# Kernel tuning notes

Hardware: AMD Instinct MI355X
Metric: run time of the kernel (lower is better)

## Reference

```python
import jax, jax.numpy as jnp
import numpy as np

EPS = 1e-5
H = 12  # num_heads

def ste_sign(x):
    # forward: sign(x) in {-1,+1}; backward: grad passes where |x|<1 (clip STE)
    c = jnp.clip(x, -1.0, 1.0)
    s = jnp.where(x >= 0, 1.0, -1.0).astype(x.dtype)
    return c + jax.lax.stop_gradient(s - c)

def bin_w(w):
    # adaptive per-output-channel scaling: alpha = mean|w| (detached), weight = alpha*sign(w)
    alpha = jax.lax.stop_gradient(jnp.mean(jnp.abs(w), axis=1, keepdims=True))
    return alpha * ste_sign(w)

def layernorm(x, g, b):
    mu = jnp.mean(x, axis=-1, keepdims=True)
    var = jnp.var(x, axis=-1, keepdims=True)
    return (x - mu) * jax.lax.rsqrt(var + EPS) * g + b

def setup_inputs():
    key = jax.random.key(0)
    ks = jax.random.split(key, 6)
    B, N, C, hid = 8, 1024, 768, 3072
    s = 0.02
    return {
        "x": jax.random.normal(ks[0], (B, N, C), jnp.float32),
        "ln1_g": jnp.ones((C,), jnp.float32),
        "ln1_b": jnp.zeros((C,), jnp.float32),
        "w_qkv": jax.random.normal(ks[1], (3 * C, C), jnp.float32) * s,
        "w_proj": jax.random.normal(ks[2], (C, C), jnp.float32) * s,
        "b_proj": jnp.zeros((C,), jnp.float32),
        "ls1_g": 1e-5 * jnp.ones((C,), jnp.float32),
        "ln2_g": jnp.ones((C,), jnp.float32),
        "ln2_b": jnp.zeros((C,), jnp.float32),
        "w_fc1": jax.random.normal(ks[3], (hid, C), jnp.float32) * s,
        "b_fc1": jnp.zeros((hid,), jnp.float32),
        "w_fc2": jax.random.normal(ks[4], (C, hid), jnp.float32) * s,
        "b_fc2": jnp.zeros((C,), jnp.float32),
        "ls2_g": 1e-5 * jnp.ones((C,), jnp.float32),
    }

def reference(x, ln1_g, ln1_b, w_qkv, w_proj, b_proj, ls1_g, ln2_g, ln2_b, w_fc1, b_fc1, w_fc2, b_fc2, ls2_g):
    B, N, C = x.shape
    hd = C // H
    scale = hd ** -0.5
    # --- binarized attention ---
    h = layernorm(x, ln1_g, ln1_b)
    qkv = jnp.einsum('bnc,oc->bno', ste_sign(h), bin_w(w_qkv))        # 1w1a qkv proj
    qkv = qkv.reshape(B, N, 3, H, hd).transpose(2, 0, 3, 1, 4)        # [3,B,H,N,hd]
    bqkv = ste_sign(qkv)                                              # BinaryQuantizer
    q, k, v = bqkv[0], bqkv[1], bqkv[2]
    attn = jnp.einsum('bhnd,bhmd->bhnm', q, k) * scale                # [B,H,N,N]
    sm = jax.nn.softmax(attn, axis=-1)
    abin = (attn > 0).astype(x.dtype)                                 # SoftmaxBinaryQuantizer fwd value
    attn_eff = sm + jax.lax.stop_gradient(abin - sm)                  # STE: fwd=binary, bwd=softmax
    o = jnp.einsum('bhnm,bhmd->bhnd', attn_eff, v)
    o = o.transpose(0, 2, 1, 3).reshape(B, N, C)
    o = jnp.einsum('bnc,oc->bno', ste_sign(o), bin_w(w_proj)) + b_proj
    x = x + ls1_g * o
    # --- binary MLP (1-bit weight, 32-bit activation) ---
    h2 = layernorm(x, ln2_g, ln2_b)
    m = jax.nn.gelu(jnp.einsum('bnc,hc->bnh', h2, bin_w(w_fc1)) + b_fc1, approximate=False)
    m = jnp.einsum('bnh,ch->bnc', m, bin_w(w_fc2)) + b_fc2
    return x + ls2_g * m
```

## Files before the change

kernel.cpp:

```cpp
#include <hip/hip_runtime.h>

#define NTOK 8192
#define CDIM 768
#define HIDD 3072
#define NQKV 2304
#define SEQL 1024
#define NHEAD 12

typedef int i32x4 __attribute__((ext_vector_type(4)));
typedef signed char sc16 __attribute__((ext_vector_type(16)));

__device__ __forceinline__ void gload_lds16(const void* g, void* l) {
    __builtin_amdgcn_global_load_lds(
        (const __attribute__((address_space(1))) unsigned int*)g,
        (__attribute__((address_space(3))) unsigned int*)l, 16, 0, 0);
}

__global__ void sign_w_kernel(const float* __restrict__ w, signed char* __restrict__ ws, int n) {
    int i = blockIdx.x * blockDim.x + threadIdx.x;
    int stride = gridDim.x * blockDim.x;
    for (; i < n; i += stride)
        ws[i] = (w[i] >= 0.0f) ? 1 : -1;
}

__global__ void __launch_bounds__(256) signalpha_kernel(const float* __restrict__ w,
                                                        signed char* __restrict__ ws,
                                                        float* __restrict__ alpha, int K) {
    int row = blockIdx.x;
    const float* wr = w + (size_t)row * K;
    signed char* wsr = ws + (size_t)row * K;
    float s = 0.f;
    for (int i = threadIdx.x; i < K; i += 256) {
        float v = wr[i];
        wsr[i] = (v >= 0.f) ? 1 : -1;
        s += fabsf(v);
    }
    for (int off = 32; off > 0; off >>= 1) s += __shfl_down(s, off);
    __shared__ float red[4];
    if ((threadIdx.x & 63) == 0) red[threadIdx.x >> 6] = s;
    __syncthreads();
    if (threadIdx.x == 0) alpha[row] = (red[0] + red[1] + red[2] + red[3]) / (float)K;
}

__global__ void __launch_bounds__(256) ln_sign_kernel(const float* __restrict__ x, const float* __restrict__ g,
                                                      const float* __restrict__ b, signed char* __restrict__ out) {
    int row = blockIdx.x;
    const float* xr = x + (size_t)row * CDIM;
    float v0 = xr[threadIdx.x], v1 = xr[threadIdx.x + 256], v2 = xr[threadIdx.x + 512];
    float s = v0 + v1 + v2, s2 = v0 * v0 + v1 * v1 + v2 * v2;
    for (int off = 32; off > 0; off >>= 1) { s += __shfl_down(s, off); s2 += __shfl_down(s2, off); }
    __shared__ float red[8];
    if ((threadIdx.x & 63) == 0) { red[threadIdx.x >> 6] = s; red[4 + (threadIdx.x >> 6)] = s2; }
    __syncthreads();
    float ts = red[0] + red[1] + red[2] + red[3];
    float t2 = red[4] + red[5] + red[6] + red[7];
    float mu = ts * (1.0f / CDIM);
    float var = t2 * (1.0f / CDIM) - mu * mu;
    float rstd = rsqrtf(var + 1e-5f);
    signed char* orow = out + (size_t)row * CDIM;
    float vv[3] = {v0, v1, v2};
#pragma unroll
    for (int p = 0; p < 3; p++) {
        int i = threadIdx.x + p * 256;
        float val = (vv[p] - mu) * rstd * g[i] + b[i];
        orow[i] = (val >= 0.f) ? 1 : -1;
    }
}

__global__ void __launch_bounds__(256) ln2q_kernel(const float* __restrict__ x, const float* __restrict__ g,
                                                   const float* __restrict__ b, signed char* __restrict__ out,
                                                   float* __restrict__ rowscale) {
    int row = blockIdx.x;
    const float* xr = x + (size_t)row * CDIM;
    float v0 = xr[threadIdx.x], v1 = xr[threadIdx.x + 256], v2 = xr[threadIdx.x + 512];
    float s = v0 + v1 + v2, s2 = v0 * v0 + v1 * v1 + v2 * v2;
    for (int off = 32; off > 0; off >>= 1) { s += __shfl_down(s, off); s2 += __shfl_down(s2, off); }
    __shared__ float red[8];
    __shared__ float redm[4];
    if ((threadIdx.x & 63) == 0) { red[threadIdx.x >> 6] = s; red[4 + (threadIdx.x >> 6)] = s2; }
    __syncthreads();
    float ts = red[0] + red[1] + red[2] + red[3];
    float t2 = red[4] + red[5] + red[6] + red[7];
    float mu = ts * (1.0f / CDIM);
    float var = t2 * (1.0f / CDIM) - mu * mu;
    float rstd = rsqrtf(var + 1e-5f);
    float a0 = (v0 - mu) * rstd * g[threadIdx.x] + b[threadIdx.x];
    float a1 = (v1 - mu) * rstd * g[threadIdx.x + 256] + b[threadIdx.x + 256];
    float a2v = (v2 - mu) * rstd * g[threadIdx.x + 512] + b[threadIdx.x + 512];
    float mx = fmaxf(fabsf(a0), fmaxf(fabsf(a1), fabsf(a2v)));
    for (int off = 32; off > 0; off >>= 1) mx = fmaxf(mx, __shfl_down(mx, off));
    if ((threadIdx.x & 63) == 0) redm[threadIdx.x >> 6] = mx;
    __syncthreads();
    float rmax = fmaxf(fmaxf(redm[0], redm[1]), fmaxf(redm[2], redm[3]));
    rmax = fmaxf(rmax, 1e-20f);
    float inv = 127.f / rmax;
    signed char* orow = out + (size_t)row * CDIM;
    orow[threadIdx.x]       = (signed char)__float2int_rn(a0 * inv);
    orow[threadIdx.x + 256] = (signed char)__float2int_rn(a1 * inv);
    orow[threadIdx.x + 512] = (signed char)__float2int_rn(a2v * inv);
    if (threadIdx.x == 0) rowscale[row] = rmax * (1.f / 127.f);
}

enum { EPI_SIGN = 0, EPI_RESID = 1, EPI_GELU = 2, EPI_QKV = 3 };
#define MSCALE_INV 16.0f

template<int EPI, int BN>
__global__ void __launch_bounds__(256) gemm_i8(
    const signed char* __restrict__ A, const signed char* __restrict__ B,
    int M, int N, int K,
    const float* __restrict__ alpha, const float* __restrict__ bias,
    const float* __restrict__ ls, const float* __restrict__ resid,
    const float* __restrict__ rowscale, float ascale,
    float* __restrict__ outF, signed char* __restrict__ outB,
    signed char* __restrict__ vtB)
{
    __shared__ signed char As[3][128][64];
    __shared__ signed char Bs[3][BN][64];
    const int tid = threadIdx.x, ln = tid & 63, w = tid >> 6;
    const int wm = w >> 1, wn = w & 1;
    const int lq = ln & 15, khi = ln >> 4;
    constexpr int NF = BN / 32;
    constexpr int L = (BN == 128) ? 4 : 3;

    const int nwg = gridDim.x * gridDim.y;
    const int id = blockIdx.y * gridDim.x + blockIdx.x;
    const int nid = (id & 7) * (nwg >> 3) + (id >> 3);
    const int bxs = nid % gridDim.x, bys = nid / gridDim.x;
    const int bm = bys * 128, bn = bxs * BN;

    const i32x4 iz = {0, 0, 0, 0};
    i32x4 acc[4][NF];
#pragma unroll
    for (int m = 0; m < 4; m++)
#pragma unroll
        for (int n = 0; n < NF; n++) acc[m][n] = iz;

    const int srow = tid >> 2, scol = (tid & 3) * 16;
    const int ssrc = ((tid & 3) ^ ((srow >> 1) & 3)) * 16;
    const int sa = 16 * (khi ^ ((lq >> 1) & 3));

    auto STAGE = [&](int p, int k0) {
        gload_lds16(A + (size_t)(bm + srow) * K + k0 + ssrc, &As[p][srow][scol]);
        gload_lds16(A + (size_t)(bm + 64 + srow) * K + k0 + ssrc, &As[p][64 + srow][scol]);
        gload_lds16(B + (size_t)(bn + srow) * K + k0 + ssrc, &Bs[p][srow][scol]);
        if constexpr (BN == 128)
            gload_lds16(B + (size_t)(bn + 64 + srow) * K + k0 + ssrc, &Bs[p][64 + srow][scol]);
    };
    auto COMPUTE = [&](int p, bool prefetch, int knext) {
        i32x4 aF[4], bF[NF];
#pragma unroll
        for (int m = 0; m < 4; m++) aF[m] = *(const i32x4*)&As[p][wm * 64 + m * 16 + lq][sa];
#pragma unroll
        for (int n = 0; n < NF; n++) bF[n] = *(const i32x4*)&Bs[p][wn * (BN / 2) + n * 16 + lq][sa];
        if (prefetch) STAGE((p + 2) % 3, knext);
        __builtin_amdgcn_s_setprio(1);
#pragma unroll
        for (int m = 0; m < 4; m++)
#pragma unroll
            for (int n = 0; n < NF; n++)
                acc[m][n] = __builtin_amdgcn_mfma_i32_16x16x64_i8(aF[m], bF[n], acc[m][n], 0, 0, 0);
        __builtin_amdgcn_s_setprio(0);
    };

    const int nst = K >> 6;
    STAGE(0, 0);
    STAGE(1, 64);
#pragma unroll 1
    for (int t = 0; t < nst - 1; t++) {
        asm volatile("s_waitcnt vmcnt(%0)" :: "n"(L) : "memory");
        __builtin_amdgcn_s_barrier();
        COMPUTE(t % 3, t + 2 < nst, (t + 2) << 6);
    }
    asm volatile("s_waitcnt vmcnt(0)" ::: "memory");
    __builtin_amdgcn_s_barrier();
    COMPUTE((nst - 1) % 3, false, 0);

    const int r0 = bm + wm * 64, c0 = bn + wn * (BN / 2);
#pragma unroll
    for (int m = 0; m < 4; m++) {
#pragma unroll
        for (int n = 0; n < NF; n++) {
            int c = c0 + n * 16 + lq;
#pragma unroll
            for (int i = 0; i < 4; i++) {
                int r = r0 + m * 16 + khi * 4 + i;
                int v = acc[m][n][i];
                if (EPI == EPI_SIGN) {
                    outB[(size_t)r * N + c] = (v >= 0) ? 1 : -1;
                } else if (EPI == EPI_RESID) {
                    float t = alpha[c] * ((float)v * ascale) + bias[c];
                    size_t idx = (size_t)r * N + c;
                    outF[idx] = resid[idx] + ls[c] * t;
                } else if (EPI == EPI_GELU) {
                    float t = alpha[c] * ((float)v * rowscale[r]) + bias[c];
                    float y2 = 1.5957691f * t + 0.07135481f * t * t * t;
                    float ge = t * __builtin_amdgcn_rcpf(1.0f + __expf(-y2));
                    float qf = fminf(fmaxf(ge * MSCALE_INV, -127.f), 127.f);
                    outB[(size_t)r * N + c] = (signed char)__float2int_rn(qf);
                }
            }
            if (EPI == EPI_QKV) {
                if (c < 1536) {
#pragma unroll
                    for (int i = 0; i < 4; i++) {
                        int r = r0 + m * 16 + khi * 4 + i;
                        outB[(size_t)r * 1536 + c] = (acc[m][n][i] >= 0) ? 1 : -1;
                    }
                } else {
                    int rb = r0 + m * 16 + khi * 4;
                    int hh = (c - 1536) >> 6, dd = (c - 1536) & 63;
                    unsigned pk = 0;
#pragma unroll
                    for (int i = 0; i < 4; i++)
                        pk |= (unsigned)(unsigned char)((acc[m][n][i] >= 0) ? 1 : -1) << (8 * i);
                    *(unsigned*)(vtB + (((size_t)(rb >> 10) * NHEAD + hh) * 64 + dd) * SEQL + (rb & 1023)) = pk;
                }
            }
        }
    }
}

__global__ void __launch_bounds__(256) attn_v2(const signed char* __restrict__ qk,
                                               const signed char* __restrict__ vt,
                                               signed char* __restrict__ a2) {
    const int id = blockIdx.x;
    const int nid = (id & 7) * 96 + (id >> 3);
    const int bh = nid >> 3, qb = nid & 7;
    const int b = bh / NHEAD, h = bh % NHEAD;
    const int tid = threadIdx.x, ln = tid & 63, w = tid >> 6;
    const int lq = ln & 15, khi = ln >> 4;

    __shared__ signed char Ks[64][80];
    __shared__ signed char Vts[64][80];
    __shared__ signed char Pw[4][32][80];

    const size_t tokbase = (size_t)b * SEQL;
    const int q0 = qb * 128 + w * 32;
    const int str = tid >> 2, stc = (tid & 3) * 16;
    const size_t vtrow = ((size_t)bh * 64 + str) * SEQL;

    i32x4 qfrag[2];
#pragma unroll
    for (int qf = 0; qf < 2; qf++)
        qfrag[qf] = *(const i32x4*)(qk + (tokbase + q0 + qf * 16 + lq) * 1536 + h * 64 + khi * 16);

    const i32x4 iz = {0, 0, 0, 0};
    i32x4 o[2][4];
#pragma unroll
    for (int qf = 0; qf < 2; qf++)
#pragma unroll
        for (int df = 0; df < 4; df++) o[qf][df] = iz;

    auto LOADJ = [&](int j, sc16& kr, sc16& vr) {
        kr = *(const sc16*)(qk + (tokbase + j * 64 + str) * 1536 + 768 + h * 64 + stc);
        vr = *(const sc16*)(vt + vtrow + j * 64 + stc);
    };
    auto STORE = [&](const sc16& kr, const sc16& vr) {
        *(sc16*)&Ks[str][stc] = kr;
        *(sc16*)&Vts[str][stc] = vr;
    };
    auto COMPUTE = [&]() {
        i32x4 kfrag[4];
#pragma unroll
        for (int kf = 0; kf < 4; kf++)
            kfrag[kf] = *(const i32x4*)&Ks[kf * 16 + lq][khi * 16];
#pragma unroll
        for (int kf = 0; kf < 4; kf++) {
#pragma unroll
            for (int qf = 0; qf < 2; qf++) {
                i32x4 st = __builtin_amdgcn_mfma_i32_16x16x64_i8(kfrag[kf], qfrag[qf], iz, 0, 0, 0);
                unsigned pb = (st[0] > 0 ? 1u : 0u) | (st[1] > 0 ? 0x100u : 0u) |
                              (st[2] > 0 ? 0x10000u : 0u) | (st[3] > 0 ? 0x1000000u : 0u);
                *(unsigned*)&Pw[w][qf * 16 + lq][kf * 16 + khi * 4] = pb;
            }
        }
        i32x4 pa[2];
#pragma unroll
        for (int qf = 0; qf < 2; qf++)
            pa[qf] = *(const i32x4*)&Pw[w][qf * 16 + lq][khi * 16];
#pragma unroll
        for (int df = 0; df < 4; df++) {
            i32x4 vfr = *(const i32x4*)&Vts[df * 16 + lq][khi * 16];
#pragma unroll
            for (int qf = 0; qf < 2; qf++)
                o[qf][df] = __builtin_amdgcn_mfma_i32_16x16x64_i8(pa[qf], vfr, o[qf][df], 0, 0, 0);
        }
    };

    sc16 ka, va, kb, vb;
    LOADJ(0, ka, va);
#pragma unroll 1
    for (int jj = 0; jj < 16; jj += 2) {
        __syncthreads();
        STORE(ka, va);
        __syncthreads();
        LOADJ(jj + 1, kb, vb);
        COMPUTE();
        __syncthreads();
        STORE(kb, vb);
        __syncthreads();
        if (jj + 2 < 16) LOADJ(jj + 2, ka, va);
        COMPUTE();
    }

#pragma unroll
    for (int qf = 0; qf < 2; qf++)
#pragma unroll
        for (int df = 0; df < 4; df++)
#pragma unroll
            for (int i = 0; i < 4; i++) {
                int qrow = q0 + qf * 16 + khi * 4 + i;
                int dim = df * 16 + lq;
                a2[(tokbase + qrow) * CDIM + h * 64 + dim] = (o[qf][df][i] >= 0) ? 1 : -1;
            }
}

static const size_t OFF_WQKV  = 0;
static const size_t OFF_WPROJ = 1769472;
static const size_t OFF_WFC1  = 2359296;
static const size_t OFF_WFC2  = 4718592;
static const size_t OFF_APROJ = 7077888;
static const size_t OFF_AFC1  = 7080960;
static const size_t OFF_AFC2  = 7093248;
static const size_t OFF_H2SC  = 7096320;
static const size_t OFF_QK    = 7129088;
static const size_t OFF_VT    = 19712000;
static const size_t OFF_A2    = 26003456;
static const size_t OFF_A1    = 32294912;
static const size_t OFF_M1    = 38586368;
static const size_t OFF_H2    = 63752192;

extern "C" void kernel_launch(void* const* d_in, const int* in_sizes, int n_in,
                              void* d_out, int out_size, void* d_ws, size_t ws_size,
                              hipStream_t stream) {
    const float* x      = (const float*)d_in[0];
    const float* ln1_g  = (const float*)d_in[1];
    const float* ln1_b  = (const float*)d_in[2];
    const float* w_qkv  = (const float*)d_in[3];
    const float* w_proj = (const float*)d_in[4];
    const float* b_proj = (const float*)d_in[5];
    const float* ls1_g  = (const float*)d_in[6];
    const float* ln2_g  = (const float*)d_in[7];
    const float* ln2_b  = (const float*)d_in[8];
    const float* w_fc1  = (const float*)d_in[9];
    const float* b_fc1  = (const float*)d_in[10];
    const float* w_fc2  = (const float*)d_in[11];
    const float* b_fc2  = (const float*)d_in[12];
    const float* ls2_g  = (const float*)d_in[13];
    float* out = (float*)d_out;

    char* ws = (char*)d_ws;
    signed char* wqkv_s  = (signed char*)(ws + OFF_WQKV);
    signed char* wproj_s = (signed char*)(ws + OFF_WPROJ);
    signed char* wfc1_s  = (signed char*)(ws + OFF_WFC1);
    signed char* wfc2_s  = (signed char*)(ws + OFF_WFC2);
    float* a_proj  = (float*)(ws + OFF_APROJ);
    float* a_fc1   = (float*)(ws + OFF_AFC1);
    float* a_fc2   = (float*)(ws + OFF_AFC2);
    float* h2scale = (float*)(ws + OFF_H2SC);
    signed char* qk   = (signed char*)(ws + OFF_QK);
    signed char* vt   = (signed char*)(ws + OFF_VT);
    signed char* a2   = (signed char*)(ws + OFF_A2);
    signed char* a1   = (signed char*)(ws + OFF_A1);
    signed char* m1   = (signed char*)(ws + OFF_M1);
    signed char* h2   = (signed char*)(ws + OFF_H2);

    sign_w_kernel<<<512, 256, 0, stream>>>(w_qkv, wqkv_s, NQKV * CDIM);
    signalpha_kernel<<<CDIM, 256, 0, stream>>>(w_proj, wproj_s, a_proj, CDIM);
    signalpha_kernel<<<HIDD, 256, 0, stream>>>(w_fc1,  wfc1_s,  a_fc1,  CDIM);
    signalpha_kernel<<<CDIM, 256, 0, stream>>>(w_fc2,  wfc2_s,  a_fc2,  HIDD);

    ln_sign_kernel<<<NTOK, 256, 0, stream>>>(x, ln1_g, ln1_b, a1);

    gemm_i8<EPI_QKV, 128><<<dim3(NQKV / 128, NTOK / 128), 256, 0, stream>>>(
        a1, wqkv_s, NTOK, NQKV, CDIM, nullptr, nullptr, nullptr, nullptr, nullptr, 1.0f, nullptr, qk, vt);

    attn_v2<<<768, 256, 0, stream>>>(qk, vt, a2);

    gemm_i8<EPI_RESID, 64><<<dim3(CDIM / 64, NTOK / 128), 256, 0, stream>>>(
        a2, wproj_s, NTOK, CDIM, CDIM, a_proj, b_proj, ls1_g, x, nullptr, 1.0f, out, nullptr, nullptr);

    ln2q_kernel<<<NTOK, 256, 0, stream>>>(out, ln2_g, ln2_b, h2, h2scale);

    gemm_i8<EPI_GELU, 128><<<dim3(HIDD / 128, NTOK / 128), 256, 0, stream>>>(
        h2, wfc1_s, NTOK, HIDD, CDIM, a_fc1, b_fc1, nullptr, nullptr, h2scale, 1.0f, nullptr, m1, nullptr);

    gemm_i8<EPI_RESID, 64><<<dim3(CDIM / 64, NTOK / 128), 256, 0, stream>>>(
        m1, wfc2_s, NTOK, CDIM, HIDD, a_fc2, b_fc2, ls2_g, out, nullptr, 1.0f / MSCALE_INV, out, nullptr, nullptr);
}
```

Baseline: 178.4 us.

## Pack int8 epilogue stores and stage residual epilogue through LDS for vector access

The GEMM epilogues for QKV and GELU now pack four int8 outputs into one 32-bit store per lane instead of four byte stores. The attention output does the same. This relies on a column permutation, so the K dimension of the downstream proj and fc2 weights is permuted at sign-extraction time to match the packed activation layout. The residual epilogue stages accumulators through LDS, reusing the pipeline buffers, so it can do coalesced float4 loads and stores of the residual and output. This cuts scattered narrow global writes, at the cost of an extra LDS round trip and barriers, and it depends on the permutations staying consistent.

```diff
diff --git a/kernel.cpp b/kernel.cpp
--- a/kernel.cpp
+++ b/kernel.cpp
@@ -8,6 +8,7 @@
 #define NHEAD 12
 
 typedef int i32x4 __attribute__((ext_vector_type(4)));
+typedef float f32x4 __attribute__((ext_vector_type(4)));
 typedef signed char sc16 __attribute__((ext_vector_type(16)));
 
 __device__ __forceinline__ void gload_lds16(const void* g, void* l) {
@@ -23,6 +24,7 @@
         ws[i] = (w[i] >= 0.0f) ? 1 : -1;
 }
 
+template<bool PERM>
 __global__ void __launch_bounds__(256) signalpha_kernel(const float* __restrict__ w,
                                                         signed char* __restrict__ ws,
                                                         float* __restrict__ alpha, int K) {
@@ -32,7 +34,8 @@
     float s = 0.f;
     for (int i = threadIdx.x; i < K; i += 256) {
         float v = wr[i];
-        wsr[i] = (v >= 0.f) ? 1 : -1;
+        int ip = PERM ? ((i & ~63) | (((i & 15) << 2) | ((i >> 4) & 3))) : i;
+        wsr[ip] = (v >= 0.f) ? 1 : -1;
         s += fabsf(v);
     }
     for (int off = 32; off > 0; off >>= 1) s += __shfl_down(s, off);
@@ -101,7 +104,7 @@
     if (threadIdx.x == 0) rowscale[row] = rmax * (1.f / 127.f);
 }
 
-enum { EPI_SIGN = 0, EPI_RESID = 1, EPI_GELU = 2, EPI_QKV = 3 };
+enum { EPI_RESID = 1, EPI_GELU = 2, EPI_QKV = 3 };
 #define MSCALE_INV 16.0f
 
 template<int EPI, int BN>
@@ -114,8 +117,12 @@
     float* __restrict__ outF, signed char* __restrict__ outB,
     signed char* __restrict__ vtB)
 {
-    __shared__ signed char As[3][128][64];
-    __shared__ signed char Bs[3][BN][64];
+    constexpr int STAGE_B = 3 * (128 + BN) * 64;
+    static_assert(STAGE_B >= 128 * 68 * 4 || EPI != EPI_RESID, "epi lds fits");
+    __shared__ __align__(16) char lds_raw[STAGE_B];
+    auto As = (signed char (*)[128][64])lds_raw;
+    auto Bs = (signed char (*)[BN][64])(lds_raw + 3 * 128 * 64);
+
     const int tid = threadIdx.x, ln = tid & 63, w = tid >> 6;
     const int wm = w >> 1, wn = w & 1;
     const int lq = ln & 15, khi = ln >> 4;
@@ -175,47 +182,84 @@
     __builtin_amdgcn_s_barrier();
     COMPUTE((nst - 1) % 3, false, 0);
 
-    const int r0 = bm + wm * 64, c0 = bn + wn * (BN / 2);
-#pragma unroll
-    for (int m = 0; m < 4; m++) {
+    const int r0 = bm + wm * 64, c0loc = wn * (BN / 2);
+
+    if constexpr (EPI == EPI_RESID) {
+        __syncthreads();
+        float (*Cf)[68] = (float (*)[68])lds_raw;
+#pragma unroll
+        for (int m = 0; m < 4; m++)
+#pragma unroll
+            for (int n = 0; n < NF; n++)
+#pragma unroll
+                for (int i = 0; i < 4; i++)
+                    Cf[wm * 64 + m * 16 + khi * 4 + i][c0loc + n * 16 + lq] =
+                        (float)acc[m][n][i] * ascale;
+        __syncthreads();
+#pragma unroll
+        for (int p = 0; p < 8; p++) {
+            int idx = p * 256 + tid;
+            int row = idx >> 4, c4 = (idx & 15) * 4;
+            f32x4 a4 = *(const f32x4*)&alpha[bn + c4];
+            f32x4 b4 = *(const f32x4*)&bias[bn + c4];
+            f32x4 l4 = *(const f32x4*)&ls[bn + c4];
+            f32x4 v4 = *(const f32x4*)&Cf[row][c4];
+            size_t g = (size_t)(bm + row) * N + bn + c4;
+            f32x4 r4 = *(const f32x4*)&resid[g];
+            f32x4 o4 = r4 + l4 * (a4 * v4 + b4);
+            *(f32x4*)&outF[g] = o4;
+        }
+    } else if constexpr (EPI == EPI_GELU) {
+        float al[NF], bi[NF];
 #pragma unroll
         for (int n = 0; n < NF; n++) {
-            int c = c0 + n * 16 + lq;
+            int c = bn + c0loc + n * 16 + lq;
+            al[n] = alpha[c]; bi[n] = bias[c];
+        }
+#pragma unroll
+        for (int m = 0; m < 4; m++)
 #pragma unroll
             for (int i = 0; i < 4; i++) {
                 int r = r0 + m * 16 + khi * 4 + i;
-                int v = acc[m][n][i];
-                if (EPI == EPI_SIGN) {
-                    outB[(size_t)r * N + c] = (v >= 0) ? 1 : -1;
-                } else if (EPI == EPI_RESID) {
-                    float t = alpha[c] * ((float)v * ascale) + bias[c];
-                    size_t idx = (size_t)r * N + c;
-                    outF[idx] = resid[idx] + ls[c] * t;
-                } else if (EPI == EPI_GELU) {
-                    float t = alpha[c] * ((float)v * rowscale[r]) + bias[c];
+                float rs = rowscale[r];
+                unsigned pk = 0;
+#pragma unroll
+                for (int n = 0; n < NF; n++) {
+                    float t = al[n] * ((float)acc[m][n][i] * rs) + bi[n];
                     float y2 = 1.5957691f * t + 0.07135481f * t * t * t;
                     float ge = t * __builtin_amdgcn_rcpf(1.0f + __expf(-y2));
                     float qf = fminf(fmaxf(ge * MSCALE_INV, -127.f), 127.f);
-                    outB[(size_t)r * N + c] = (signed char)__float2int_rn(qf);
+                    pk |= (unsigned)(unsigned char)(signed char)__float2int_rn(qf) << (8 * n);
                 }
+                *(unsigned*)(outB + (size_t)r * N + bn + c0loc + lq * 4) = pk;
             }
-            if (EPI == EPI_QKV) {
-                if (c < 1536) {
-#pragma unroll
-                    for (int i = 0; i < 4; i++) {
-                        int r = r0 + m * 16 + khi * 4 + i;
-                        outB[(size_t)r * 1536 + c] = (acc[m][n][i] >= 0) ? 1 : -1;
-                    }
-                } else {
+    } else {
+        if (bn < 1536) {
+#pragma unroll
+            for (int m = 0; m < 4; m++)
+#pragma unroll
+                for (int i = 0; i < 4; i++) {
+                    int r = r0 + m * 16 + khi * 4 + i;
+                    unsigned pk = 0;
+#pragma unroll
+                    for (int n = 0; n < NF; n++)
+                        pk |= (unsigned)(unsigned char)(signed char)((acc[m][n][i] >= 0) ? 1 : -1) << (8 * n);
+                    *(unsigned*)(outB + (size_t)r * 1536 + bn + c0loc + lq * 4) = pk;
+                }
+        } else {
+#pragma unroll
+            for (int m = 0; m < 4; m++)
+#pragma unroll
+                for (int n = 0; n < NF; n++) {
+                    int cg = bn + c0loc + n * 16 + lq - 1536;
+                    int hh = cg >> 6, dd = cg & 63;
                     int rb = r0 + m * 16 + khi * 4;
-                    int hh = (c - 1536) >> 6, dd = (c - 1536) & 63;
                     unsigned pk = 0;
 #pragma unroll
                     for (int i = 0; i < 4; i++)
-                        pk |= (unsigned)(unsigned char)((acc[m][n][i] >= 0) ? 1 : -1) << (8 * i);
+                        pk |= (unsigned)(unsigned char)(signed char)((acc[m][n][i] >= 0) ? 1 : -1) << (8 * i);
                     *(unsigned*)(vtB + (((size_t)(rb >> 10) * NHEAD + hh) * 64 + dd) * SEQL + (rb & 1023)) = pk;
                 }
-            }
         }
     }
 }
@@ -306,13 +350,14 @@
 #pragma unroll
     for (int qf = 0; qf < 2; qf++)
 #pragma unroll
-        for (int df = 0; df < 4; df++)
-#pragma unroll
-            for (int i = 0; i < 4; i++) {
-                int qrow = q0 + qf * 16 + khi * 4 + i;
-                int dim = df * 16 + lq;
-                a2[(tokbase + qrow) * CDIM + h * 64 + dim] = (o[qf][df][i] >= 0) ? 1 : -1;
-            }
+        for (int i = 0; i < 4; i++) {
+            int qrow = q0 + qf * 16 + khi * 4 + i;
+            unsigned pk = 0;
+#pragma unroll
+            for (int df = 0; df < 4; df++)
+                pk |= (unsigned)(unsigned char)(signed char)((o[qf][df][i] >= 0) ? 1 : -1) << (8 * df);
+            *(unsigned*)(a2 + (tokbase + qrow) * CDIM + h * 64 + lq * 4) = pk;
+        }
 }
 
 static const size_t OFF_WQKV  = 0;
@@ -366,9 +411,9 @@
     signed char* h2   = (signed char*)(ws + OFF_H2);
 
     sign_w_kernel<<<512, 256, 0, stream>>>(w_qkv, wqkv_s, NQKV * CDIM);
-    signalpha_kernel<<<CDIM, 256, 0, stream>>>(w_proj, wproj_s, a_proj, CDIM);
-    signalpha_kernel<<<HIDD, 256, 0, stream>>>(w_fc1,  wfc1_s,  a_fc1,  CDIM);
-    signalpha_kernel<<<CDIM, 256, 0, stream>>>(w_fc2,  wfc2_s,  a_fc2,  HIDD);
+    signalpha_kernel<true><<<CDIM, 256, 0, stream>>>(w_proj, wproj_s, a_proj, CDIM);
+    signalpha_kernel<false><<<HIDD, 256, 0, stream>>>(w_fc1,  wfc1_s,  a_fc1,  CDIM);
+    signalpha_kernel<true><<<CDIM, 256, 0, stream>>>(w_fc2,  wfc2_s,  a_fc2,  HIDD);
 
     ln_sign_kernel<<<NTOK, 256, 0, stream>>>(x, ln1_g, ln1_b, a1);
 
```

Result: faster. 170.9 us (-4.2%).
